# Kernel optimization log

Hardware: AMD Instinct MI355X
Metric: run time of the kernel (lower is better)

The kernel has to match this reference:

```python
import jax, jax.numpy as jnp
import numpy as np

B, S, HID = 4, 1024, 1024
NH, NKV, HD = 16, 8, 64
EPS = 1e-6
ROPE_BASE = 10000.0


def setup_inputs() -> dict:
    key = jax.random.key(0)
    ks = jax.random.split(key, 6)
    hidden_states = jax.random.normal(ks[0], (B, S, HID), jnp.float32)
    # RoPE tables: cos/sin of shape [B, S, HD] (half-frequency layout, duplicated)
    inv_freq = 1.0 / (ROPE_BASE ** (jnp.arange(0, HD, 2, dtype=jnp.float32) / HD))
    pos = jnp.arange(S, dtype=jnp.float32)
    freqs = pos[:, None] * inv_freq[None, :]              # [S, HD/2]
    emb = jnp.concatenate([freqs, freqs], axis=-1)         # [S, HD]
    cos = jnp.broadcast_to(jnp.cos(emb)[None], (B, S, HD))
    sin = jnp.broadcast_to(jnp.sin(emb)[None], (B, S, HD))
    # additive causal mask [B, 1, S, S]
    causal = jnp.where(jnp.tril(jnp.ones((S, S), bool)), 0.0, -1e9).astype(jnp.float32)
    attention_mask = jnp.broadcast_to(causal[None, None], (B, 1, S, S))
    sc = 0.02
    Wq = jax.random.normal(ks[1], (NH * HD, HID), jnp.float32) * sc
    Wk = jax.random.normal(ks[2], (NKV * HD, HID), jnp.float32) * sc
    Wv = jax.random.normal(ks[3], (NKV * HD, HID), jnp.float32) * sc
    Wo = jax.random.normal(ks[4], (HID, NH * HD), jnp.float32) * sc
    q_norm_w = jnp.ones((HD,), jnp.float32)
    k_norm_w = jnp.ones((HD,), jnp.float32)
    return {"hidden_states": hidden_states, "cos": cos, "sin": sin,
            "attention_mask": attention_mask, "Wq": Wq, "Wk": Wk, "Wv": Wv,
            "Wo": Wo, "q_norm_w": q_norm_w, "k_norm_w": k_norm_w}


def _rms_norm(x, w):
    dt = x.dtype
    x32 = x.astype(jnp.float32)
    var = jnp.mean(x32 * x32, axis=-1, keepdims=True)
    x32 = x32 * jax.lax.rsqrt(var + EPS)
    return w * x32.astype(dt)


def _rotate_half(x):
    x1, x2 = jnp.split(x, 2, axis=-1)
    return jnp.concatenate([-x2, x1], axis=-1)


def reference(hidden_states, cos, sin, attention_mask, Wq, Wk, Wv, Wo, q_norm_w, k_norm_w):
    b, s, _ = hidden_states.shape
    scaling = HD ** -0.5
    # QKV projections (bias=False), reshape to heads, per-head RMSNorm on q/k
    q = (hidden_states @ Wq.T).reshape(b, s, NH, HD)
    k = (hidden_states @ Wk.T).reshape(b, s, NKV, HD)
    v = (hidden_states @ Wv.T).reshape(b, s, NKV, HD)
    q = _rms_norm(q, q_norm_w).transpose(0, 2, 1, 3)   # [B, NH, S, HD]
    k = _rms_norm(k, k_norm_w).transpose(0, 2, 1, 3)   # [B, NKV, S, HD]
    v = v.transpose(0, 2, 1, 3)                         # [B, NKV, S, HD]
    # RoPE (unsqueeze_dim=1 -> broadcast over heads)
    c = cos[:, None, :, :]
    sn = sin[:, None, :, :]
    q = q * c + _rotate_half(q) * sn
    k = k * c + _rotate_half(k) * sn
    # GQA: repeat kv heads
    groups = NH // NKV
    k = jnp.repeat(k, groups, axis=1)
    v = jnp.repeat(v, groups, axis=1)
    # eager attention
    scores = jnp.einsum('bhqd,bhkd->bhqk', q, k) * scaling + attention_mask
    attn_weights = jax.nn.softmax(scores.astype(jnp.float32), axis=-1).astype(q.dtype)
    ctx = jnp.einsum('bhqk,bhkd->bhqd', attn_weights, v)
    ctx = ctx.transpose(0, 2, 1, 3).reshape(b, s, NH * HD)
    out = ctx @ Wo.T
    return (out, attn_weights)
```

## Files before the change

kernel.cpp:

```cpp
#include <hip/hip_runtime.h>
#include <hip/hip_fp16.h>

#define Bb 4
#define Ss 1024
#define HID 1024
#define NH 16
#define NKV 8
#define HD 64

typedef _Float16 f16x8 __attribute__((ext_vector_type(8)));
typedef _Float16 f16x4 __attribute__((ext_vector_type(4)));
typedef float f32x4 __attribute__((ext_vector_type(4)));

typedef const __attribute__((address_space(1))) unsigned int gu32;
typedef __attribute__((address_space(3))) unsigned int lu32;

__device__ __forceinline__ void gl_lds16(const _Float16* g, _Float16* l) {
  __builtin_amdgcn_global_load_lds((gu32*)g, (lu32*)l, 16, 0, 0);
}

__global__ __launch_bounds__(256) void f2h_all(
    const float* __restrict__ a0, const float* __restrict__ a1,
    const float* __restrict__ a2, const float* __restrict__ a3,
    const float* __restrict__ a4, _Float16* __restrict__ o0,
    _Float16* __restrict__ o1, _Float16* __restrict__ o2,
    _Float16* __restrict__ o3, _Float16* __restrict__ o4) {
  const int bid = blockIdx.x;
  const float* src;
  _Float16* dst;
  int base;
  if (bid < 4096)      { src = a0; dst = o0; base = bid; }
  else if (bid < 5120) { src = a1; dst = o1; base = bid - 4096; }
  else if (bid < 5632) { src = a2; dst = o2; base = bid - 5120; }
  else if (bid < 6144) { src = a3; dst = o3; base = bid - 5632; }
  else                 { src = a4; dst = o4; base = bid - 6144; }
  const int i = base * 1024 + threadIdx.x * 4;
  const float4 v = *(const float4*)(src + i);
  f16x4 h;
  h[0] = (_Float16)v.x; h[1] = (_Float16)v.y;
  h[2] = (_Float16)v.z; h[3] = (_Float16)v.w;
  *(f16x4*)(dst + i) = h;
}

template <int EPI>
__global__ __launch_bounds__(256) void gemm128(
    const _Float16* __restrict__ A, const _Float16* __restrict__ Bt,
    float* __restrict__ C, _Float16* __restrict__ qh, _Float16* __restrict__ kh,
    _Float16* __restrict__ vTp, const float* __restrict__ qnw,
    const float* __restrict__ knw, const float* __restrict__ cosd,
    const float* __restrict__ sind, int N, int K) {
  __shared__ __align__(16) _Float16 As[128][64];
  __shared__ __align__(16) _Float16 Bs[128][64];
  const int tid = threadIdx.x;
  const int wave = tid >> 6, lane = tid & 63;
  const int lr = lane & 15, lk = lane >> 4;
  const int wr = wave >> 1, wc = wave & 1;
  const int bm = blockIdx.x * 128;
  const int by = blockIdx.y;
  const int bn = by * 128;

  f32x4 acc[4][4] = {};

  const _Float16* asrc[4];
  const _Float16* bsrc[4];
  _Float16 *adst[4], *bdst[4];
#pragma unroll
  for (int i = 0; i < 4; ++i) {
    const int ch = i * 256 + tid;
    const int r = ch >> 3, ccl = ch & 7;
    const int ccg = ccl ^ (r & 7);
    asrc[i] = A + (size_t)(bm + r) * K + ccg * 8;
    bsrc[i] = Bt + (size_t)(bn + r) * K + ccg * 8;
    adst[i] = &As[0][0] + ch * 8;
    bdst[i] = &Bs[0][0] + ch * 8;
  }

  for (int k0 = 0; k0 < K; k0 += 64) {
    __syncthreads();
#pragma unroll
    for (int i = 0; i < 4; ++i) {
      gl_lds16(asrc[i] + k0, adst[i]);
      gl_lds16(bsrc[i] + k0, bdst[i]);
    }
    __syncthreads();
#pragma unroll
    for (int kk = 0; kk < 2; ++kk) {
      f16x8 af[4], bf[4];
#pragma unroll
      for (int m = 0; m < 4; ++m) {
        const int r = wr * 64 + m * 16 + lr;
        const int s = (kk * 4 + lk) ^ (r & 7);
        af[m] = *(const f16x8*)(&As[r][0] + s * 8);
      }
#pragma unroll
      for (int n = 0; n < 4; ++n) {
        const int r = wc * 64 + n * 16 + lr;
        const int s = (kk * 4 + lk) ^ (r & 7);
        bf[n] = *(const f16x8*)(&Bs[r][0] + s * 8);
      }
#pragma unroll
      for (int m = 0; m < 4; ++m)
#pragma unroll
        for (int n = 0; n < 4; ++n)
          acc[m][n] =
              __builtin_amdgcn_mfma_f32_16x16x32_f16(af[m], bf[n], acc[m][n], 0, 0, 0);
    }
  }

  if (EPI == 0) {
#pragma unroll
    for (int m = 0; m < 4; ++m) {
      const int row = bm + wr * 64 + m * 16 + lk * 4;
#pragma unroll
      for (int n = 0; n < 4; ++n) {
        const int c = bn + wc * 64 + n * 16 + lr;
#pragma unroll
        for (int j = 0; j < 4; ++j)
          C[(size_t)(row + j) * N + c] = acc[m][n][j];
      }
    }
  } else {
    const int b = bm >> 10;
    const int s0 = bm & 1023;
    const int hd2 = by * 2 + wc;
    if (hd2 < 24) {
      const bool isQ = (hd2 < 16);
      const float* nw = isQ ? qnw : knw;
      _Float16* dst = isQ ? qh : kh;
      const int ncols = isQ ? (NH * HD) : (NKV * HD);
      const int hcol = (isQ ? hd2 : (hd2 - 16)) * HD;
      float nwv[4];
#pragma unroll
      for (int n = 0; n < 4; ++n) nwv[n] = nw[n * 16 + lr];
#pragma unroll
      for (int m = 0; m < 4; ++m) {
#pragma unroll
        for (int j = 0; j < 4; ++j) {
          const int row = bm + wr * 64 + m * 16 + lk * 4 + j;
          float ss = 0.f;
#pragma unroll
          for (int n = 0; n < 4; ++n) ss += acc[m][n][j] * acc[m][n][j];
#pragma unroll
          for (int o = 1; o < 16; o <<= 1) ss += __shfl_xor(ss, o);
          const float rs = rsqrtf(ss * (1.0f / 64.0f) + 1e-6f);
          float y[4];
#pragma unroll
          for (int n = 0; n < 4; ++n) y[n] = acc[m][n][j] * rs * nwv[n];
          const size_t rb = (size_t)row * HD;
#pragma unroll
          for (int n = 0; n < 4; ++n) {
            const int d = n * 16 + lr;
            const float rot = (n < 2) ? -y[n + 2] : y[n - 2];
            dst[(size_t)row * ncols + hcol + d] =
                (_Float16)(y[n] * cosd[rb + d] + rot * sind[rb + d]);
          }
        }
      }
    } else {
      const int kv = hd2 - 24;
#pragma unroll
      for (int m = 0; m < 4; ++m) {
        const int sbase = s0 + wr * 64 + m * 16 + lk * 4;
#pragma unroll
        for (int n = 0; n < 4; ++n) {
          const int d = n * 16 + lr;
          f16x4 pk;
#pragma unroll
          for (int j = 0; j < 4; ++j) pk[j] = (_Float16)acc[m][n][j];
          *(f16x4*)&vTp[((size_t)((b * NKV + kv) * HD + d)) * Ss + sbase] = pk;
        }
      }
    }
  }
}

__global__ __launch_bounds__(256) void gemm_oproj(
    const _Float16* __restrict__ A, const _Float16* __restrict__ Bt,
    float* __restrict__ C, int N, int K) {
  __shared__ __align__(16) _Float16 As[128][64];
  __shared__ __align__(16) _Float16 Bs[64][64];
  const int tid = threadIdx.x;
  const int wave = tid >> 6, lane = tid & 63;
  const int lr = lane & 15, lk = lane >> 4;
  const int bm = blockIdx.x * 128;
  const int bn = blockIdx.y * 64;

  f32x4 acc[2][4] = {};

  const _Float16* asrc[4];
  const _Float16* bsrc[2];
  _Float16 *adst[4], *bdst[2];
#pragma unroll
  for (int i = 0; i < 4; ++i) {
    const int ch = i * 256 + tid;
    const int r = ch >> 3, ccl = ch & 7;
    const int ccg = ccl ^ (r & 7);
    asrc[i] = A + (size_t)(bm + r) * K + ccg * 8;
    adst[i] = &As[0][0] + ch * 8;
  }
#pragma unroll
  for (int i = 0; i < 2; ++i) {
    const int ch = i * 256 + tid;
    const int r = ch >> 3, ccl = ch & 7;
    const int ccg = ccl ^ (r & 7);
    bsrc[i] = Bt + (size_t)(bn + r) * K + ccg * 8;
    bdst[i] = &Bs[0][0] + ch * 8;
  }

  for (int k0 = 0; k0 < K; k0 += 64) {
    __syncthreads();
#pragma unroll
    for (int i = 0; i < 4; ++i) gl_lds16(asrc[i] + k0, adst[i]);
#pragma unroll
    for (int i = 0; i < 2; ++i) gl_lds16(bsrc[i] + k0, bdst[i]);
    __syncthreads();
#pragma unroll
    for (int kk = 0; kk < 2; ++kk) {
      f16x8 af[2], bf[4];
#pragma unroll
      for (int m = 0; m < 2; ++m) {
        const int r = wave * 32 + m * 16 + lr;
        const int s = (kk * 4 + lk) ^ (r & 7);
        af[m] = *(const f16x8*)(&As[r][0] + s * 8);
      }
#pragma unroll
      for (int n = 0; n < 4; ++n) {
        const int r = n * 16 + lr;
        const int s = (kk * 4 + lk) ^ (r & 7);
        bf[n] = *(const f16x8*)(&Bs[r][0] + s * 8);
      }
#pragma unroll
      for (int m = 0; m < 2; ++m)
#pragma unroll
        for (int n = 0; n < 4; ++n)
          acc[m][n] =
              __builtin_amdgcn_mfma_f32_16x16x32_f16(af[m], bf[n], acc[m][n], 0, 0, 0);
    }
  }
#pragma unroll
  for (int m = 0; m < 2; ++m) {
    const int row = bm + wave * 32 + m * 16 + lk * 4;
#pragma unroll
    for (int n = 0; n < 4; ++n) {
      const int c = bn + n * 16 + lr;
#pragma unroll
      for (int j = 0; j < 4; ++j)
        C[(size_t)(row + j) * N + c] = acc[m][n][j];
    }
  }
}

__global__ __launch_bounds__(512) void attn_kernel(
    const _Float16* __restrict__ qh, const _Float16* __restrict__ kh,
    const _Float16* __restrict__ vT, float* __restrict__ attn,
    _Float16* __restrict__ ctxh) {
  __shared__ __align__(16) _Float16 Ks[64][72];
  __shared__ __align__(16) _Float16 Vs[64][72];
  __shared__ __align__(16) _Float16 Wh[8][16][72];
  const int x = blockIdx.x, g = blockIdx.y, b = blockIdx.z;
  int qt;
  switch (b) {
    case 0:  qt = x; break;
    case 1:  qt = (x + 8) & 15; break;
    case 2:  qt = 15 - x; break;
    default: qt = (7 - x) & 15; break;
  }
  const int tid = threadIdx.x, wave = tid >> 6, lane = tid & 63;
  const int lr = lane & 15, lk = lane >> 4;
  const int h = 2 * g + (wave >> 2);
  const int q0 = qt * 64, qrow0 = q0 + (wave & 3) * 16;
  float* attn_bh = attn + (size_t)(b * NH + h) * Ss * Ss;

  const int sr = tid >> 3, sc = tid & 7;
  const _Float16* kb0 = kh + (size_t)(b * Ss) * (NKV * HD) + g * HD + sc * 8;
  const _Float16* vb0 = vT + (size_t)((b * NKV + g) * HD) * Ss + sc * 8;

  const _Float16* qp = qh + (size_t)(b * Ss + qrow0 + lr) * (NH * HD) + h * HD + lk * 8;
  const f16x8 aq0 = *(const f16x8*)qp;
  const f16x8 aq1 = *(const f16x8*)(qp + 32);

  const float C1 = 0.18033688011112042f;
  const float C2 = -11.541560327111707f;

  f16x8 pk = *(const f16x8*)(kb0 + (size_t)sr * (NKV * HD));
  float lsum[4] = {0.f, 0.f, 0.f, 0.f};
  for (int t = 0; t <= qt; ++t) {
    __syncthreads();
    *(f16x8*)&Ks[sr][sc * 8] = pk;
    if (t < qt)
      pk = *(const f16x8*)(kb0 + (size_t)((t + 1) * 64 + sr) * (NKV * HD));
    __syncthreads();
    f32x4 acc[4] = {};
#pragma unroll
    for (int n = 0; n < 4; ++n) {
      f16x8 b0 = *(const f16x8*)&Ks[n * 16 + lr][lk * 8];
      acc[n] = __builtin_amdgcn_mfma_f32_16x16x32_f16(aq0, b0, acc[n], 0, 0, 0);
    }
#pragma unroll
    for (int n = 0; n < 4; ++n) {
      f16x8 b1 = *(const f16x8*)&Ks[n * 16 + lr][32 + lk * 8];
      acc[n] = __builtin_amdgcn_mfma_f32_16x16x32_f16(aq1, b1, acc[n], 0, 0, 0);
    }
    if (t < qt) {
#pragma unroll
      for (int j = 0; j < 4; ++j)
#pragma unroll
        for (int n = 0; n < 4; ++n) lsum[j] += exp2f(fmaf(acc[n][j], C1, C2));
    } else {
#pragma unroll
      for (int j = 0; j < 4; ++j) {
        const int gr = qrow0 + lk * 4 + j;
#pragma unroll
        for (int n = 0; n < 4; ++n) {
          float p = exp2f(fmaf(acc[n][j], C1, C2));
          if (q0 + n * 16 + lr > gr) p = 0.f;
          lsum[j] += p;
        }
      }
    }
  }
  float linv[4];
#pragma unroll
  for (int j = 0; j < 4; ++j) {
#pragma unroll
    for (int o = 1; o < 16; o <<= 1) lsum[j] += __shfl_xor(lsum[j], o);
    linv[j] = 1.0f / lsum[j];
  }

  pk = *(const f16x8*)(kb0 + (size_t)sr * (NKV * HD));
  f16x8 pv = *(const f16x8*)(vb0 + (size_t)sr * Ss);
  f32x4 acc2[4] = {};
  const int wr2 = lane >> 4;
  const int wc2 = (lane & 15) * 4;
  for (int t = 0; t <= qt; ++t) {
    __syncthreads();
    *(f16x8*)&Ks[sr][sc * 8] = pk;
    *(f16x8*)&Vs[sr][sc * 8] = pv;
    if (t < qt) {
      pk = *(const f16x8*)(kb0 + (size_t)((t + 1) * 64 + sr) * (NKV * HD));
      pv = *(const f16x8*)(vb0 + (size_t)sr * Ss + (t + 1) * 64);
    }
    __syncthreads();
    f32x4 acc[4] = {};
#pragma unroll
    for (int n = 0; n < 4; ++n) {
      f16x8 b0 = *(const f16x8*)&Ks[n * 16 + lr][lk * 8];
      acc[n] = __builtin_amdgcn_mfma_f32_16x16x32_f16(aq0, b0, acc[n], 0, 0, 0);
    }
#pragma unroll
    for (int n = 0; n < 4; ++n) {
      f16x8 b1 = *(const f16x8*)&Ks[n * 16 + lr][32 + lk * 8];
      acc[n] = __builtin_amdgcn_mfma_f32_16x16x32_f16(aq1, b1, acc[n], 0, 0, 0);
    }
    if (t < qt) {
#pragma unroll
      for (int j = 0; j < 4; ++j)
#pragma unroll
        for (int n = 0; n < 4; ++n) {
          const float w = exp2f(fmaf(acc[n][j], C1, C2)) * linv[j];
          Wh[wave][lk * 4 + j][n * 16 + lr] = (_Float16)w;
        }
    } else {
#pragma unroll
      for (int j = 0; j < 4; ++j) {
        const int gr = qrow0 + lk * 4 + j;
#pragma unroll
        for (int n = 0; n < 4; ++n) {
          float w = exp2f(fmaf(acc[n][j], C1, C2)) * linv[j];
          if (q0 + n * 16 + lr > gr) w = 0.f;
          Wh[wave][lk * 4 + j][n * 16 + lr] = (_Float16)w;
        }
      }
    }
#pragma unroll
    for (int kc = 0; kc < 2; ++kc) {
      f16x8 aw = *(const f16x8*)&Wh[wave][lr][kc * 32 + lk * 8];
#pragma unroll
      for (int n = 0; n < 4; ++n) {
        f16x8 bv = *(const f16x8*)&Vs[n * 16 + lr][kc * 32 + lk * 8];
        acc2[n] = __builtin_amdgcn_mfma_f32_16x16x32_f16(aw, bv, acc2[n], 0, 0, 0);
      }
    }
#pragma unroll
    for (int i2 = 0; i2 < 4; ++i2) {
      f16x4 hv = *(const f16x4*)&Wh[wave][wr2 + i2 * 4][wc2];
      *(float4*)&attn_bh[(size_t)(qrow0 + wr2 + i2 * 4) * Ss + t * 64 + wc2] =
          make_float4((float)hv[0], (float)hv[1], (float)hv[2], (float)hv[3]);
    }
  }

  {
    float* attn_z = attn + (size_t)(b * NH + 2 * g + (tid >> 8)) * Ss * Ss;
    const int tz = tid & 255;
    for (int t = qt + 1; t < 16; ++t)
      for (int idx = tz; idx < 1024; idx += 256) {
        int r = idx >> 4, c4 = (idx & 15) * 4;
        *(float4*)&attn_z[(size_t)(q0 + r) * Ss + t * 64 + c4] =
            make_float4(0.f, 0.f, 0.f, 0.f);
      }
  }

#pragma unroll
  for (int n = 0; n < 4; ++n)
#pragma unroll
    for (int j = 0; j < 4; ++j)
      ctxh[(size_t)(b * Ss + qrow0 + lk * 4 + j) * (NH * HD) + h * HD + n * 16 + lr] =
          (_Float16)acc2[n][j];
}

extern "C" void kernel_launch(void* const* d_in, const int* in_sizes, int n_in,
                              void* d_out, int out_size, void* d_ws, size_t ws_size,
                              hipStream_t stream) {
  const float* hs   = (const float*)d_in[0];
  const float* cosb = (const float*)d_in[1];
  const float* sinb = (const float*)d_in[2];
  const float* Wq = (const float*)d_in[4];
  const float* Wk = (const float*)d_in[5];
  const float* Wv = (const float*)d_in[6];
  const float* Wo = (const float*)d_in[7];
  const float* qw = (const float*)d_in[8];
  const float* kw = (const float*)d_in[9];

  char* ws = (char*)d_ws;
  _Float16* Xh    = (_Float16*)(ws);
  _Float16* Wqkvh = (_Float16*)(ws + 8388608);
  _Float16* Woh   = (_Float16*)(ws + 12582912);
  _Float16* qh    = (_Float16*)(ws + 14680064);
  _Float16* kh    = (_Float16*)(ws + 23068672);
  _Float16* vT    = (_Float16*)(ws + 27262976);
  _Float16* ctxh  = (_Float16*)(ws + 31457280);

  float* out  = (float*)d_out;
  float* attn = out + (size_t)Bb * Ss * HID;

  f2h_all<<<7168, 256, 0, stream>>>(hs, Wq, Wk, Wv, Wo, Xh, Wqkvh,
                                    Wqkvh + 1048576, Wqkvh + 1572864, Woh);

  gemm128<1><<<dim3(32, 16), 256, 0, stream>>>(
      Xh, Wqkvh, nullptr, qh, kh, vT, qw, kw, cosb, sinb, 2048, 1024);

  attn_kernel<<<dim3(16, 8, 4), 512, 0, stream>>>(qh, kh, vT, attn, ctxh);

  gemm_oproj<<<dim3(32, 16), 256, 0, stream>>>(ctxh, Woh, out, 1024, 1024);
}
```

Measured before the change: 128.5 us.

## Use 128x64 tiles for QKV GEMM and stage ctx stores through LDS

The fused QKV projection kernel drops its template and moves from 128x128 to 128x64 output tiles, so each block covers exactly one head. This doubles the grid to 1024 blocks for better CU occupancy and simplifies the norm/RoPE/V-transpose epilogue. The attention kernel now stages its fp16 context output in a shared tile and writes it as 16-byte vector stores instead of scattered 2-byte stores. The trade-off is more total A-tile traffic, since each A tile is loaded by twice as many blocks.

```diff
diff --git a/kernel.cpp b/kernel.cpp
--- a/kernel.cpp
+++ b/kernel.cpp
@@ -42,64 +42,68 @@
   *(f16x4*)(dst + i) = h;
 }
 
-template <int EPI>
-__global__ __launch_bounds__(256) void gemm128(
+__global__ __launch_bounds__(256) void gemm_qkv(
     const _Float16* __restrict__ A, const _Float16* __restrict__ Bt,
-    float* __restrict__ C, _Float16* __restrict__ qh, _Float16* __restrict__ kh,
+    _Float16* __restrict__ qh, _Float16* __restrict__ kh,
     _Float16* __restrict__ vTp, const float* __restrict__ qnw,
     const float* __restrict__ knw, const float* __restrict__ cosd,
-    const float* __restrict__ sind, int N, int K) {
-  __shared__ __align__(16) _Float16 As[128][64];
-  __shared__ __align__(16) _Float16 Bs[128][64];
+    const float* __restrict__ sind) {
+  const int K = 1024;
+  __shared__ __align__(16) _Float16 As[128 * 64];
+  __shared__ __align__(16) _Float16 Bs[64 * 64];
   const int tid = threadIdx.x;
   const int wave = tid >> 6, lane = tid & 63;
   const int lr = lane & 15, lk = lane >> 4;
-  const int wr = wave >> 1, wc = wave & 1;
   const int bm = blockIdx.x * 128;
   const int by = blockIdx.y;
-  const int bn = by * 128;
-
-  f32x4 acc[4][4] = {};
+  const int bn = by * 64;
+
+  f32x4 acc[2][4] = {};
 
   const _Float16* asrc[4];
-  const _Float16* bsrc[4];
-  _Float16 *adst[4], *bdst[4];
+  const _Float16* bsrc[2];
+  _Float16 *adst[4], *bdst[2];
 #pragma unroll
   for (int i = 0; i < 4; ++i) {
     const int ch = i * 256 + tid;
     const int r = ch >> 3, ccl = ch & 7;
     const int ccg = ccl ^ (r & 7);
     asrc[i] = A + (size_t)(bm + r) * K + ccg * 8;
+    adst[i] = As + ch * 8;
+  }
+#pragma unroll
+  for (int i = 0; i < 2; ++i) {
+    const int ch = i * 256 + tid;
+    const int r = ch >> 3, ccl = ch & 7;
+    const int ccg = ccl ^ (r & 7);
     bsrc[i] = Bt + (size_t)(bn + r) * K + ccg * 8;
-    adst[i] = &As[0][0] + ch * 8;
-    bdst[i] = &Bs[0][0] + ch * 8;
+    bdst[i] = Bs + ch * 8;
   }
 
   for (int k0 = 0; k0 < K; k0 += 64) {
     __syncthreads();
 #pragma unroll
-    for (int i = 0; i < 4; ++i) {
-      gl_lds16(asrc[i] + k0, adst[i]);
-      gl_lds16(bsrc[i] + k0, bdst[i]);
-    }
+    for (int i = 0; i < 4; ++i) gl_lds16(asrc[i] + k0, adst[i]);
+#pragma unroll
+    for (int i = 0; i < 2; ++i) gl_lds16(bsrc[i] + k0, bdst[i]);
     __syncthreads();
 #pragma unroll
     for (int kk = 0; kk < 2; ++kk) {
-      f16x8 af[4], bf[4];
-#pragma unroll
-      for (int m = 0; m < 4; ++m) {
-        const int r = wr * 64 + m * 16 + lr;
+      f16x8 af[2], bf[4];
+#pragma unroll
+      for (int m = 0; m < 2; ++m) {
+        const int r = wave * 32 + m * 16 + lr;
         const int s = (kk * 4 + lk) ^ (r & 7);
-        af[m] = *(const f16x8*)(&As[r][0] + s * 8);
+        af[m] = *(const f16x8*)(As + r * 64 + s * 8);
       }
 #pragma unroll
       for (int n = 0; n < 4; ++n) {
-        const int r = wc * 64 + n * 16 + lr;
+        const int r = n * 16 + lr;
         const int s = (kk * 4 + lk) ^ (r & 7);
-        bf[n] = *(const f16x8*)(&Bs[r][0] + s * 8);
-      }
-#pragma unroll
-      for (int m = 0; m < 4; ++m)
+        bf[n] = *(const f16x8*)(Bs + r * 64 + s * 8);
+      }
+#pragma unroll
+      for (int m = 0; m < 2; ++m)
 #pragma unroll
         for (int n = 0; n < 4; ++n)
           acc[m][n] =
@@ -107,68 +111,53 @@
     }
   }
 
-  if (EPI == 0) {
-#pragma unroll
-    for (int m = 0; m < 4; ++m) {
-      const int row = bm + wr * 64 + m * 16 + lk * 4;
-#pragma unroll
-      for (int n = 0; n < 4; ++n) {
-        const int c = bn + wc * 64 + n * 16 + lr;
-#pragma unroll
-        for (int j = 0; j < 4; ++j)
-          C[(size_t)(row + j) * N + c] = acc[m][n][j];
-      }
-    }
-  } else {
-    const int b = bm >> 10;
-    const int s0 = bm & 1023;
-    const int hd2 = by * 2 + wc;
-    if (hd2 < 24) {
-      const bool isQ = (hd2 < 16);
-      const float* nw = isQ ? qnw : knw;
-      _Float16* dst = isQ ? qh : kh;
-      const int ncols = isQ ? (NH * HD) : (NKV * HD);
-      const int hcol = (isQ ? hd2 : (hd2 - 16)) * HD;
-      float nwv[4];
-#pragma unroll
-      for (int n = 0; n < 4; ++n) nwv[n] = nw[n * 16 + lr];
-#pragma unroll
-      for (int m = 0; m < 4; ++m) {
-#pragma unroll
-        for (int j = 0; j < 4; ++j) {
-          const int row = bm + wr * 64 + m * 16 + lk * 4 + j;
-          float ss = 0.f;
-#pragma unroll
-          for (int n = 0; n < 4; ++n) ss += acc[m][n][j] * acc[m][n][j];
-#pragma unroll
-          for (int o = 1; o < 16; o <<= 1) ss += __shfl_xor(ss, o);
-          const float rs = rsqrtf(ss * (1.0f / 64.0f) + 1e-6f);
-          float y[4];
-#pragma unroll
-          for (int n = 0; n < 4; ++n) y[n] = acc[m][n][j] * rs * nwv[n];
-          const size_t rb = (size_t)row * HD;
-#pragma unroll
-          for (int n = 0; n < 4; ++n) {
-            const int d = n * 16 + lr;
-            const float rot = (n < 2) ? -y[n + 2] : y[n - 2];
-            dst[(size_t)row * ncols + hcol + d] =
-                (_Float16)(y[n] * cosd[rb + d] + rot * sind[rb + d]);
-          }
-        }
-      }
-    } else {
-      const int kv = hd2 - 24;
-#pragma unroll
-      for (int m = 0; m < 4; ++m) {
-        const int sbase = s0 + wr * 64 + m * 16 + lk * 4;
+  const int b = bm >> 10;
+  const int s0 = bm & 1023;
+  if (by < 24) {
+    const bool isQ = (by < 16);
+    const float* nw = isQ ? qnw : knw;
+    _Float16* dst = isQ ? qh : kh;
+    const int ncols = isQ ? (NH * HD) : (NKV * HD);
+    const int hcol = (isQ ? by : (by - 16)) * HD;
+    float nwv[4];
+#pragma unroll
+    for (int n = 0; n < 4; ++n) nwv[n] = nw[n * 16 + lr];
+#pragma unroll
+    for (int m = 0; m < 2; ++m) {
+#pragma unroll
+      for (int j = 0; j < 4; ++j) {
+        const int row = bm + wave * 32 + m * 16 + lk * 4 + j;
+        float ss = 0.f;
+#pragma unroll
+        for (int n = 0; n < 4; ++n) ss += acc[m][n][j] * acc[m][n][j];
+#pragma unroll
+        for (int o = 1; o < 16; o <<= 1) ss += __shfl_xor(ss, o);
+        const float rs = rsqrtf(ss * (1.0f / 64.0f) + 1e-6f);
+        float y[4];
+#pragma unroll
+        for (int n = 0; n < 4; ++n) y[n] = acc[m][n][j] * rs * nwv[n];
+        const size_t rb = (size_t)row * HD;
 #pragma unroll
         for (int n = 0; n < 4; ++n) {
           const int d = n * 16 + lr;
-          f16x4 pk;
-#pragma unroll
-          for (int j = 0; j < 4; ++j) pk[j] = (_Float16)acc[m][n][j];
-          *(f16x4*)&vTp[((size_t)((b * NKV + kv) * HD + d)) * Ss + sbase] = pk;
+          const float rot = (n < 2) ? -y[n + 2] : y[n - 2];
+          dst[(size_t)row * ncols + hcol + d] =
+              (_Float16)(y[n] * cosd[rb + d] + rot * sind[rb + d]);
         }
+      }
+    }
+  } else {
+    const int kv = by - 24;
+#pragma unroll
+    for (int m = 0; m < 2; ++m) {
+      const int sbase = s0 + wave * 32 + m * 16 + lk * 4;
+#pragma unroll
+      for (int n = 0; n < 4; ++n) {
+        const int d = n * 16 + lr;
+        f16x4 pk;
+#pragma unroll
+        for (int j = 0; j < 4; ++j) pk[j] = (_Float16)acc[m][n][j];
+        *(f16x4*)&vTp[((size_t)((b * NKV + kv) * HD + d)) * Ss + sbase] = pk;
       }
     }
   }
@@ -404,8 +393,14 @@
   for (int n = 0; n < 4; ++n)
 #pragma unroll
     for (int j = 0; j < 4; ++j)
-      ctxh[(size_t)(b * Ss + qrow0 + lk * 4 + j) * (NH * HD) + h * HD + n * 16 + lr] =
-          (_Float16)acc2[n][j];
+      Wh[wave][lk * 4 + j][n * 16 + lr] = (_Float16)acc2[n][j];
+#pragma unroll
+  for (int i = 0; i < 2; ++i) {
+    const int cid = i * 64 + lane;
+    const int r3 = cid >> 3, c3 = cid & 7;
+    f16x8 cv = *(const f16x8*)&Wh[wave][r3][c3 * 8];
+    *(f16x8*)&ctxh[(size_t)(b * Ss + qrow0 + r3) * (NH * HD) + h * HD + c3 * 8] = cv;
+  }
 }
 
 extern "C" void kernel_launch(void* const* d_in, const int* in_sizes, int n_in,
@@ -436,8 +431,8 @@
   f2h_all<<<7168, 256, 0, stream>>>(hs, Wq, Wk, Wv, Wo, Xh, Wqkvh,
                                     Wqkvh + 1048576, Wqkvh + 1572864, Woh);
 
-  gemm128<1><<<dim3(32, 16), 256, 0, stream>>>(
-      Xh, Wqkvh, nullptr, qh, kh, vT, qw, kw, cosb, sinb, 2048, 1024);
+  gemm_qkv<<<dim3(32, 32), 256, 0, stream>>>(Xh, Wqkvh, qh, kh, vT, qw, kw,
+                                             cosb, sinb);
 
   attn_kernel<<<dim3(16, 8, 4), 512, 0, stream>>>(qh, kh, vT, attn, ctxh);
 
```

Result: faster. 124.8 us (median of 2 runs) (-2.9%).
